# Kernel tuning notes

Hardware: AMD Instinct MI355X
Metric: run time of the kernel (lower is better)

The kernel has to match this reference:

```python
import jax, jax.numpy as jnp
import numpy as np

N_NODES = 50000
N_EDGES = 1600000
IN_DIM = 128
HID = 64
EPS = 1e-6


def setup_inputs() -> dict:
    key = jax.random.key(0)
    ks = jax.random.split(key, 12)
    def g(k, shape, scale):
        return jax.random.normal(k, shape, dtype=jnp.float32) * scale
    x = g(ks[0], (N_NODES, IN_DIM), 1.0)
    edge_index = jax.random.randint(ks[1], (2, N_EDGES), 0, N_NODES, dtype=jnp.int64)
    return {
        "x": x,
        "edge_index": edge_index,
        "w0s": g(ks[2], (IN_DIM, HID), 1.0 / np.sqrt(IN_DIM)),
        "w0n": g(ks[3], (IN_DIM, HID), 1.0 / np.sqrt(IN_DIM)),
        "w1s": g(ks[4], (HID, HID), 1.0 / np.sqrt(HID)),
        "w1n": g(ks[5], (HID, HID), 1.0 / np.sqrt(HID)),
        "w2s": g(ks[6], (HID, HID), 1.0 / np.sqrt(HID)),
        "w2n": g(ks[7], (HID, HID), 1.0 / np.sqrt(HID)),
        "mw1": g(ks[8], (HID, 32), 1.0 / np.sqrt(HID)),
        "mb1": jnp.zeros((32,), jnp.float32),
        "mw2": g(ks[9], (32, 1), 1.0 / np.sqrt(32.0)),
        "mb2": jnp.zeros((1,), jnp.float32),
    }


def _uhg_layer(h, src, dst, inv_deg, ws, wn):
    # transform-then-gather (cheaper: GEMM at node granularity, gather at edge granularity)
    msg = (h @ wn)[src]                                    # [E, HID]
    agg = jax.ops.segment_sum(msg, dst, num_segments=N_NODES) * inv_deg  # mean over in-neighbors
    h2 = jax.nn.relu(h @ ws + agg)
    # projective (UHG) normalization: map embedding back onto the unit sphere / projective rep
    return h2 / (jnp.linalg.norm(h2, axis=-1, keepdims=True) + EPS)


def reference(x, edge_index, w0s, w0n, w1s, w1n, w2s, w2n, mw1, mb1, mw2, mb2):
    src, dst = edge_index[0], edge_index[1]
    deg = jax.ops.segment_sum(jnp.ones((N_EDGES,), jnp.float32), dst, num_segments=N_NODES)
    inv_deg = (1.0 / jnp.maximum(deg, 1.0))[:, None]       # [N,1]
    h = _uhg_layer(x, src, dst, inv_deg, w0s, w0n)
    h = _uhg_layer(h, src, dst, inv_deg, w1s, w1n)
    h = _uhg_layer(h, src, dst, inv_deg, w2s, w2n)
    h = jax.nn.relu(h @ mw1 + mb1)                         # [N,32]
    return jax.nn.sigmoid(h @ mw2 + mb2)                   # [N,1]
```

## Files before the change

kernel.cpp:

```cpp
#include <hip/hip_runtime.h>
#include <hip/hip_bf16.h>
#include <math.h>

#define N_NODES 50000
#define N_EDGES 1600000
#define IN_DIM  128
#define HID     64
#define EPB     4096
#define NBLK    391
#define NB      391
#define CAP     8192
static constexpr float EPS = 1e-6f;

typedef __attribute__((ext_vector_type(8))) short          short8;
typedef __attribute__((ext_vector_type(8))) unsigned short ushort8;
typedef __attribute__((ext_vector_type(4))) float          f32x4;
typedef __attribute__((ext_vector_type(2))) float          f32x2;

__device__ __forceinline__ float bf2f(unsigned int hi_bits) {
    union { unsigned int i; float f; } c; c.i = hi_bits; return c.f;
}
__device__ __forceinline__ unsigned short f2bf(float f) {
    union { float f; unsigned int i; } c; c.f = f;
    unsigned int r = c.i + 0x7FFFu + ((c.i >> 16) & 1u);
    return (unsigned short)(r >> 16);
}
__device__ __forceinline__ unsigned char f2fp8(float f) {
    int p = __builtin_amdgcn_cvt_pk_fp8_f32(f, f, 0, false);
    return (unsigned char)(p & 0xff);
}


template <int K>
__device__ __forceinline__ void pack_body(const float* __restrict__ wS,
                                          const float* __restrict__ wN,
                                          unsigned short* __restrict__ pS,
                                          unsigned short* __restrict__ pN, int blk) {
    constexpr int NSLOT = (K / 32) * 4 * 64;
    int slot = blk * 256 + (int)threadIdx.x;
    if (slot >= NSLOT) return;
    int lane = slot & 63;
    int ct   = slot >> 6;
    int t    = ct & 3;
    int c    = ct >> 2;
    int m    = lane & 15;
    int quad = lane >> 4;
    int col  = t * 16 + m;
#pragma unroll
    for (int j = 0; j < 8; ++j) {
        int k = c * 32 + quad * 8 + j;
        pS[slot * 8 + j] = f2bf(wS[k * 64 + col]);
        pN[slot * 8 + j] = f2bf(wN[k * 64 + col]);
    }
}


__global__ __launch_bounds__(256) void bucket_count_pack(
    const int* __restrict__ ei, int* __restrict__ blockCounts,
    const float* __restrict__ w0s, const float* __restrict__ w0n,
    const float* __restrict__ w1s, const float* __restrict__ w1n,
    const float* __restrict__ w2s, const float* __restrict__ w2n,
    unsigned short* __restrict__ p0S, unsigned short* __restrict__ p0N,
    unsigned short* __restrict__ p1S, unsigned short* __restrict__ p1N,
    unsigned short* __restrict__ p2S, unsigned short* __restrict__ p2N,
    unsigned char* __restrict__ hnq) {
    if (blockIdx.x >= NBLK) {
        int blk = blockIdx.x - NBLK;
        if (blk == 7 && threadIdx.x >= 128 && threadIdx.x < 144)
            ((unsigned int*)(hnq + (size_t)N_NODES * HID))[threadIdx.x - 128] = 0u;
        if (blk < 4)      pack_body<IN_DIM>(w0s, w0n, p0S, p0N, blk);
        else if (blk < 6) pack_body<HID>(w1s, w1n, p1S, p1N, blk - 4);
        else              pack_body<HID>(w2s, w2n, p2S, p2N, blk - 6);
        return;
    }
    __shared__ int hist[NB];
    for (int i = threadIdx.x; i < NB; i += 256) hist[i] = 0;
    __syncthreads();
    int base = blockIdx.x * EPB;
    int lim  = min(EPB, N_EDGES - base);
    for (int i = threadIdx.x; i < lim; i += 256)
        atomicAdd(&hist[ei[N_EDGES + base + i] >> 7], 1);
    __syncthreads();
    for (int b = threadIdx.x; b < NB; b += 256)
        blockCounts[blockIdx.x * NB + b] = hist[b];
}

template <int K, bool F32IN>
__device__ __forceinline__ void gemm_body(
    const void* __restrict__ Av,
    const unsigned short* __restrict__ pS,
    const unsigned short* __restrict__ pN,
    float* __restrict__ hs, unsigned char* __restrict__ hnq, int blk) {
    constexpr int NC = K / 32;
    int lane = threadIdx.x & 63;
    int wv   = threadIdx.x >> 6;
    int tile = blk * 4 + wv;
    if (tile >= N_NODES / 16) return;
    int m    = lane & 15;
    int quad = lane >> 4;

    const short8* pSf = (const short8*)pS;
    const short8* pNf = (const short8*)pN;

    f32x4 accS[4], accN[4];
#pragma unroll
    for (int t = 0; t < 4; ++t) {
        accS[t] = (f32x4){0.f, 0.f, 0.f, 0.f};
        accN[t] = (f32x4){0.f, 0.f, 0.f, 0.f};
    }
#pragma unroll
    for (int c = 0; c < NC; ++c) {
        short8 a;
        if constexpr (F32IN) {
            const float* Af = (const float*)Av + ((size_t)tile * 16 + m) * K + quad * 8 + c * 32;
            f32x4 a0 = *(const f32x4*)Af;
            f32x4 a1 = *(const f32x4*)(Af + 4);
#pragma unroll
            for (int k = 0; k < 4; ++k) a[k]     = (short)f2bf(a0[k]);
#pragma unroll
            for (int k = 0; k < 4; ++k) a[k + 4] = (short)f2bf(a1[k]);
        } else {
            const short8* Af = (const short8*)((const unsigned short*)Av +
                               ((size_t)tile * 16 + m) * K + quad * 8);
            a = Af[c * 4];
        }
#pragma unroll
        for (int t = 0; t < 4; ++t) {
            short8 bs = pSf[(c * 4 + t) * 64 + lane];
            short8 bn = pNf[(c * 4 + t) * 64 + lane];
            accS[t] = __builtin_amdgcn_mfma_f32_16x16x32_bf16(a, bs, accS[t], 0, 0, 0);
            accN[t] = __builtin_amdgcn_mfma_f32_16x16x32_bf16(a, bn, accN[t], 0, 0, 0);
        }
    }
    int row0 = tile * 16 + quad * 4;
#pragma unroll
    for (int t = 0; t < 4; ++t) {
#pragma unroll
        for (int r = 0; r < 4; ++r) {
            size_t o = (size_t)(row0 + r) * HID + t * 16 + m;
            hs[o]  = accS[t][r];
            hnq[o] = f2fp8(accN[t][r]);
        }
    }
}

__global__ __launch_bounds__(256) void col_sum_gemm0(
    const int* __restrict__ blockCounts, int* __restrict__ totals,
    const float* __restrict__ x,
    const unsigned short* __restrict__ p0S, const unsigned short* __restrict__ p0N,
    float* __restrict__ hs, unsigned char* __restrict__ hnq) {
    if (blockIdx.x >= NB) {
        gemm_body<IN_DIM, true>(x, p0S, p0N, hs, hnq, blockIdx.x - NB);
        return;
    }
    __shared__ int ws[4];
    int b = blockIdx.x;
    int s = 0;
    for (int i = threadIdx.x; i < NBLK; i += 256) s += blockCounts[i * NB + b];
#pragma unroll
    for (int off = 32; off >= 1; off >>= 1) s += __shfl_xor(s, off, 64);
    if ((threadIdx.x & 63) == 0) ws[threadIdx.x >> 6] = s;
    __syncthreads();
    if (threadIdx.x == 0) totals[b] = ws[0] + ws[1] + ws[2] + ws[3];
}

__global__ __launch_bounds__(256) void col_fix_base(int* __restrict__ blockCounts,
                                                    const int* __restrict__ totals,
                                                    int* __restrict__ bucketBase) {
    __shared__ int vals[NBLK];
    __shared__ int sbase;
    int b = blockIdx.x;
    for (int i = threadIdx.x; i < NBLK; i += 256) vals[i] = blockCounts[i * NB + b];
    if (threadIdx.x < 64) {
        int lane = threadIdx.x;
        int s = 0;
        for (int i = lane; i < b; i += 64) s += totals[i];
#pragma unroll
        for (int off = 32; off >= 1; off >>= 1) s += __shfl_xor(s, off, 64);
        if (lane == 0) {
            sbase = s;
            bucketBase[b] = s;
            if (b == NB - 1) bucketBase[NB] = s + totals[b];
        }
    }
    __syncthreads();
    if (threadIdx.x < 64) {
        int lane  = threadIdx.x;
        int carry = sbase;
        for (int base = 0; base < NBLK; base += 64) {
            int i = base + lane;
            int v = (i < NBLK) ? vals[i] : 0;
            int incl = v;
#pragma unroll
            for (int off = 1; off < 64; off <<= 1) {
                int t = __shfl_up(incl, off, 64);
                if (lane >= off) incl += t;
            }
            if (i < NBLK) vals[i] = carry + incl - v;
            carry += __shfl(incl, 63, 64);
        }
    }
    __syncthreads();
    for (int i = threadIdx.x; i < NBLK; i += 256) blockCounts[i * NB + b] = vals[i];
}

__global__ __launch_bounds__(256) void bucket_scatter(const int* __restrict__ ei,
                                                      const int* __restrict__ blockCounts,
                                                      unsigned int* __restrict__ bucketPacked) {
    __shared__ int cur[NB];
    for (int b = threadIdx.x; b < NB; b += 256)
        cur[b] = blockCounts[blockIdx.x * NB + b];
    __syncthreads();
    int base = blockIdx.x * EPB;
    int lim  = min(EPB, N_EDGES - base);
    for (int i = threadIdx.x; i < lim; i += 256) {
        int s = ei[base + i];
        int d = ei[N_EDGES + base + i];
        int pos = atomicAdd(&cur[d >> 7], 1);
        bucketPacked[pos] = ((unsigned int)s << 7) | (unsigned int)(d & 127);
    }
}

__global__ __launch_bounds__(256) void node_scan_scatter(
    const unsigned int* __restrict__ bucketPacked, const int* __restrict__ bucketBase,
    int* __restrict__ rowptr, int* __restrict__ csr_src) {
    __shared__ int cnt[128];
    __shared__ int half0;
    __shared__ unsigned int stage[CAP];
    int tid = threadIdx.x;
    if (tid < 128) cnt[tid] = 0;
    __syncthreads();
    int beg = bucketBase[blockIdx.x], end = bucketBase[blockIdx.x + 1];
    int n = end - beg;
    for (int i = tid; i < n; i += 256) {
        unsigned int e = bucketPacked[beg + i];
        if (i < CAP) stage[i] = e;
        atomicAdd(&cnt[e & 127], 1);
    }
    __syncthreads();
    int lane = tid & 63;
    int v    = (tid < 128) ? cnt[tid] : 0;
    int incl = v;
#pragma unroll
    for (int off = 1; off < 64; off <<= 1) {
        int t = __shfl_up(incl, off, 64);
        if (lane >= off) incl += t;
    }
    if (tid == 63) half0 = incl;
    __syncthreads();
    int base  = beg + ((tid >= 64 && tid < 128) ? half0 : 0);
    int start = base + incl - v;
    int node  = blockIdx.x * 128 + tid;
    if (tid < 128) {
        if (node < N_NODES) rowptr[node] = start;
        cnt[tid] = start;
    }
    if (blockIdx.x == 0 && tid == 128) rowptr[N_NODES] = N_EDGES;
    __syncthreads();
    for (int i = tid; i < n; i += 256) {
        unsigned int e = (i < CAP) ? stage[i] : bucketPacked[beg + i];
        int pos = atomicAdd(&cnt[e & 127], 1);
        csr_src[pos] = (int)(e >> 7);
    }
}

template <int K, bool F32IN>
__global__ __launch_bounds__(256) void gemm_dual_mfma(
    const void* __restrict__ Av,
    const unsigned short* __restrict__ pS,
    const unsigned short* __restrict__ pN,
    float* __restrict__ hs, unsigned char* __restrict__ hnq) {
    gemm_body<K, F32IN>(Av, pS, pN, hs, hnq, blockIdx.x);
}

template <bool MLP>
__global__ __launch_bounds__(256) void agg_update(
    const int* __restrict__ rowptr, const int* __restrict__ csr_src,
    const unsigned char* __restrict__ hnq, const float* __restrict__ hs,
    unsigned short* __restrict__ hb_out,
    const float* __restrict__ mw1, const float* __restrict__ mb1,
    const float* __restrict__ mw2, const float* __restrict__ mb2,
    float* __restrict__ out) {
    __shared__ float sW1[MLP ? HID * 32 : 1];
    __shared__ float sW2[MLP ? 32 : 1];
    __shared__ float sB1[MLP ? 32 : 1];
    __shared__ float sH[MLP ? 32 * 68 : 1];
    if (MLP) {
        for (int i = threadIdx.x; i < HID * 32; i += 256) sW1[i] = mw1[i];
        if (threadIdx.x < 32) { sW2[threadIdx.x] = mw2[threadIdx.x]; sB1[threadIdx.x] = mb1[threadIdx.x]; }
        __syncthreads();
    }
    int wid   = blockIdx.x * 4 + (threadIdx.x >> 6);
    int lane  = threadIdx.x & 63;
    int grp   = lane >> 3;
    int r     = lane & 7;
    int node  = wid * 8 + grp;
    bool valid = node < N_NODES;
    int nclamp = valid ? node : 0;
    int beg = rowptr[nclamp];
    int end = rowptr[nclamp + 1];
    int deg = end - beg;
    const unsigned char* hnqB = hnq;
    unsigned r8 = (unsigned)(r * 8);

    f32x2 acc2[4];
#pragma unroll
    for (int k = 0; k < 4; ++k) acc2[k] = (f32x2){0.f, 0.f};

    for (int t = 0; t < deg; t += 8) {
        const int* ip = csr_src + beg + t;
        int si[8];
#pragma unroll
        for (int u = 0; u < 8; ++u) {
            int vraw = ip[u];
            si[u] = (t + u < deg) ? vraw : N_NODES;
        }
        uint2 w[8];
#pragma unroll
        for (int u = 0; u < 8; ++u) {
            unsigned off = ((unsigned)si[u] << 6) | r8;
            w[u] = *(const uint2*)(hnqB + off);
        }
#pragma unroll
        for (int u = 0; u < 8; ++u) {
#if __has_builtin(__builtin_amdgcn_cvt_pk_f32_fp8)
            acc2[0] += __builtin_amdgcn_cvt_pk_f32_fp8((int)w[u].x, false);
            acc2[1] += __builtin_amdgcn_cvt_pk_f32_fp8((int)w[u].x, true);
            acc2[2] += __builtin_amdgcn_cvt_pk_f32_fp8((int)w[u].y, false);
            acc2[3] += __builtin_amdgcn_cvt_pk_f32_fp8((int)w[u].y, true);
#else
            acc2[0] += (f32x2){__builtin_amdgcn_cvt_f32_fp8((int)w[u].x, 0),
                               __builtin_amdgcn_cvt_f32_fp8((int)w[u].x, 1)};
            acc2[1] += (f32x2){__builtin_amdgcn_cvt_f32_fp8((int)w[u].x, 2),
                               __builtin_amdgcn_cvt_f32_fp8((int)w[u].x, 3)};
            acc2[2] += (f32x2){__builtin_amdgcn_cvt_f32_fp8((int)w[u].y, 0),
                               __builtin_amdgcn_cvt_f32_fp8((int)w[u].y, 1)};
            acc2[3] += (f32x2){__builtin_amdgcn_cvt_f32_fp8((int)w[u].y, 2),
                               __builtin_amdgcn_cvt_f32_fp8((int)w[u].y, 3)};
#endif
        }
    }

    float acc[8];
#pragma unroll
    for (int k = 0; k < 4; ++k) { acc[2 * k] = acc2[k][0]; acc[2 * k + 1] = acc2[k][1]; }
    float invdeg = 1.0f / fmaxf((float)deg, 1.0f);
    const float* hsr = hs + (size_t)nclamp * HID + r * 8;
    f32x4 h0 = *(const f32x4*)hsr;
    f32x4 h1 = *(const f32x4*)(hsr + 4);
    float v[8], ss = 0.f;
#pragma unroll
    for (int k = 0; k < 8; ++k) {
        float hk = (k < 4) ? h0[k] : h1[k - 4];
        v[k] = fmaxf(fmaf(acc[k], invdeg, hk), 0.f);
        ss += v[k] * v[k];
    }
    ss += __shfl_xor(ss, 1, 64);
    ss += __shfl_xor(ss, 2, 64);
    ss += __shfl_xor(ss, 4, 64);
    float rs = 1.0f / (sqrtf(ss) + EPS);
    if (MLP) {
        int sn = threadIdx.x >> 3;
#pragma unroll
        for (int k = 0; k < 8; ++k) sH[sn * 68 + r * 8 + k] = v[k] * rs;
        __syncthreads();
        int c0 = r * 4;
        float y0 = sB1[c0], y1 = sB1[c0 + 1], y2 = sB1[c0 + 2], y3 = sB1[c0 + 3];
        const float* hrow = &sH[sn * 68];
#pragma unroll 8
        for (int k = 0; k < HID; ++k) {
            float hv = hrow[k];
            const float* wrow = &sW1[k * 32 + c0];
            y0 = fmaf(hv, wrow[0], y0);
            y1 = fmaf(hv, wrow[1], y1);
            y2 = fmaf(hv, wrow[2], y2);
            y3 = fmaf(hv, wrow[3], y3);
        }
        float p = fmaxf(y0, 0.f) * sW2[c0] + fmaxf(y1, 0.f) * sW2[c0 + 1] +
                  fmaxf(y2, 0.f) * sW2[c0 + 2] + fmaxf(y3, 0.f) * sW2[c0 + 3];
        p += __shfl_xor(p, 1, 64);
        p += __shfl_xor(p, 2, 64);
        p += __shfl_xor(p, 4, 64);
        if (r == 0 && valid) out[node] = 1.0f / (1.0f + __expf(-(p + mb2[0])));
    } else {
        if (valid) {
            ushort8 o;
#pragma unroll
            for (int k = 0; k < 8; ++k) o[k] = f2bf(v[k] * rs);
            *(ushort8*)(hb_out + (size_t)node * HID + r * 8) = o;
        }
    }
}

extern "C" void kernel_launch(void* const* d_in, const int* in_sizes, int n_in,
                              void* d_out, int out_size, void* d_ws, size_t ws_size,
                              hipStream_t stream) {
    const float* x   = (const float*)d_in[0];
    const int*   ei  = (const int*)d_in[1];
    const float* w0s = (const float*)d_in[2];
    const float* w0n = (const float*)d_in[3];
    const float* w1s = (const float*)d_in[4];
    const float* w1n = (const float*)d_in[5];
    const float* w2s = (const float*)d_in[6];
    const float* w2n = (const float*)d_in[7];
    const float* mw1 = (const float*)d_in[8];
    const float* mb1 = (const float*)d_in[9];
    const float* mw2 = (const float*)d_in[10];
    const float* mb2 = (const float*)d_in[11];
    float*       out = (float*)d_out;

    int* rowptr      = (int*)d_ws;
    int* csr_src     = rowptr + 50432;
    int* blockCounts = csr_src + N_EDGES;
    int* bucketBase  = blockCounts + 153600;
    int* totals      = bucketBase + 512;
    unsigned int* bucketPacked = (unsigned int*)(totals + 512);
    const size_t NH = (size_t)N_NODES * HID;
    float*          hs  = (float*)(bucketPacked + N_EDGES);
    unsigned char*  hnq = (unsigned char*)(hs + NH);
    unsigned short* hb  = (unsigned short*)(hnq + NH + 64);
    unsigned short* p0S = hb + NH;
    unsigned short* p0N = p0S + IN_DIM * HID;
    unsigned short* p1S = p0N + IN_DIM * HID;
    unsigned short* p1N = p1S + HID * HID;
    unsigned short* p2S = p1N + HID * HID;
    unsigned short* p2N = p2S + HID * HID;

    const int nodeGrid = (N_NODES / 8 + 3) / 4;
    const int gemmGrid = (N_NODES / 16 + 3) / 4;

    bucket_count_pack<<<NBLK + 8, 256, 0, stream>>>(
        ei, blockCounts, w0s, w0n, w1s, w1n, w2s, w2n,
        p0S, p0N, p1S, p1N, p2S, p2N, hnq);
    col_sum_gemm0<<<NB + gemmGrid, 256, 0, stream>>>(
        blockCounts, totals, x, p0S, p0N, hs, hnq);
    col_fix_base<<<NB, 256, 0, stream>>>(blockCounts, totals, bucketBase);
    bucket_scatter<<<NBLK, 256, 0, stream>>>(ei, blockCounts, bucketPacked);
    node_scan_scatter<<<NB, 256, 0, stream>>>(bucketPacked, bucketBase, rowptr, csr_src);

    agg_update<false><<<nodeGrid, 256, 0, stream>>>(
        rowptr, csr_src, hnq, hs, hb, nullptr, nullptr, nullptr, nullptr, nullptr);

    gemm_dual_mfma<HID, false><<<gemmGrid, 256, 0, stream>>>(hb, p1S, p1N, hs, hnq);
    agg_update<false><<<nodeGrid, 256, 0, stream>>>(
        rowptr, csr_src, hnq, hs, hb, nullptr, nullptr, nullptr, nullptr, nullptr);

    gemm_dual_mfma<HID, false><<<gemmGrid, 256, 0, stream>>>(hb, p2S, p2N, hs, hnq);
    agg_update<true><<<nodeGrid, 256, 0, stream>>>(
        rowptr, csr_src, hnq, hs, nullptr, mw1, mb1, mw2, mb2, out);
}
```

Baseline: 221.6 us.

## Use 16 lanes per node with 4-byte gathers and vectorized aligned index loads

Reworks the aggregation kernel to assign 16 threads per node instead of 8. Each thread gathers 4 fp8 features per neighbor instead of 8. Neighbor indices are now read as aligned 16-byte vectors starting from an 8-aligned base, with out-of-range entries masked to a dummy node. The intent is more parallelism per node and fewer scalar index loads, at the cost of twice as many threads, narrower per-lane gather loads, and an extra shuffle step. The grid now assumes N_NODES is divisible by 16, so the bounds checks are dropped.

```diff
diff --git a/kernel.cpp b/kernel.cpp
--- a/kernel.cpp
+++ b/kernel.cpp
@@ -14,6 +14,8 @@
 
 typedef __attribute__((ext_vector_type(8))) short          short8;
 typedef __attribute__((ext_vector_type(8))) unsigned short ushort8;
+typedef __attribute__((ext_vector_type(4))) unsigned short bf16x4_t;
+typedef __attribute__((ext_vector_type(4))) int            i32x4;
 typedef __attribute__((ext_vector_type(4))) float          f32x4;
 typedef __attribute__((ext_vector_type(2))) float          f32x2;
 
@@ -284,111 +286,95 @@
     __shared__ float sW1[MLP ? HID * 32 : 1];
     __shared__ float sW2[MLP ? 32 : 1];
     __shared__ float sB1[MLP ? 32 : 1];
-    __shared__ float sH[MLP ? 32 * 68 : 1];
+    __shared__ float sH[MLP ? 16 * 68 : 1];
     if (MLP) {
         for (int i = threadIdx.x; i < HID * 32; i += 256) sW1[i] = mw1[i];
         if (threadIdx.x < 32) { sW2[threadIdx.x] = mw2[threadIdx.x]; sB1[threadIdx.x] = mb1[threadIdx.x]; }
         __syncthreads();
     }
-    int wid   = blockIdx.x * 4 + (threadIdx.x >> 6);
-    int lane  = threadIdx.x & 63;
-    int grp   = lane >> 3;
-    int r     = lane & 7;
-    int node  = wid * 8 + grp;
-    bool valid = node < N_NODES;
-    int nclamp = valid ? node : 0;
-    int beg = rowptr[nclamp];
-    int end = rowptr[nclamp + 1];
+    int sn   = threadIdx.x >> 4;
+    int r    = threadIdx.x & 15;
+    int node = blockIdx.x * 16 + sn;
+    int beg = rowptr[node];
+    int end = rowptr[node + 1];
     int deg = end - beg;
-    const unsigned char* hnqB = hnq;
-    unsigned r8 = (unsigned)(r * 8);
-
-    f32x2 acc2[4];
-#pragma unroll
-    for (int k = 0; k < 4; ++k) acc2[k] = (f32x2){0.f, 0.f};
-
-    for (int t = 0; t < deg; t += 8) {
-        const int* ip = csr_src + beg + t;
+    int tbase = beg & ~7;
+    int nbat  = (end - tbase + 7) >> 3;
+    const i32x4* ip = (const i32x4*)(csr_src + tbase);
+    const unsigned char* hrow = hnq + r * 4;
+
+    f32x2 acc2[2];
+    acc2[0] = (f32x2){0.f, 0.f};
+    acc2[1] = (f32x2){0.f, 0.f};
+    int pr = tbase - beg;
+
+#pragma unroll 2
+    for (int t = 0; t < nbat; ++t) {
+        i32x4 a = ip[2 * t];
+        i32x4 b = ip[2 * t + 1];
+        int p0 = pr + 8 * t;
         int si[8];
 #pragma unroll
-        for (int u = 0; u < 8; ++u) {
-            int vraw = ip[u];
-            si[u] = (t + u < deg) ? vraw : N_NODES;
-        }
-        uint2 w[8];
-#pragma unroll
-        for (int u = 0; u < 8; ++u) {
-            unsigned off = ((unsigned)si[u] << 6) | r8;
-            w[u] = *(const uint2*)(hnqB + off);
-        }
+        for (int u = 0; u < 4; ++u) {
+            si[u]     = ((unsigned)(p0 + u)     < (unsigned)deg) ? a[u] : N_NODES;
+            si[u + 4] = ((unsigned)(p0 + 4 + u) < (unsigned)deg) ? b[u] : N_NODES;
+        }
+        unsigned wv[8];
+#pragma unroll
+        for (int u = 0; u < 8; ++u)
+            wv[u] = *(const unsigned*)(hrow + ((unsigned)si[u] << 6));
 #pragma unroll
         for (int u = 0; u < 8; ++u) {
 #if __has_builtin(__builtin_amdgcn_cvt_pk_f32_fp8)
-            acc2[0] += __builtin_amdgcn_cvt_pk_f32_fp8((int)w[u].x, false);
-            acc2[1] += __builtin_amdgcn_cvt_pk_f32_fp8((int)w[u].x, true);
-            acc2[2] += __builtin_amdgcn_cvt_pk_f32_fp8((int)w[u].y, false);
-            acc2[3] += __builtin_amdgcn_cvt_pk_f32_fp8((int)w[u].y, true);
+            acc2[0] += __builtin_amdgcn_cvt_pk_f32_fp8((int)wv[u], false);
+            acc2[1] += __builtin_amdgcn_cvt_pk_f32_fp8((int)wv[u], true);
 #else
-            acc2[0] += (f32x2){__builtin_amdgcn_cvt_f32_fp8((int)w[u].x, 0),
-                               __builtin_amdgcn_cvt_f32_fp8((int)w[u].x, 1)};
-            acc2[1] += (f32x2){__builtin_amdgcn_cvt_f32_fp8((int)w[u].x, 2),
-                               __builtin_amdgcn_cvt_f32_fp8((int)w[u].x, 3)};
-            acc2[2] += (f32x2){__builtin_amdgcn_cvt_f32_fp8((int)w[u].y, 0),
-                               __builtin_amdgcn_cvt_f32_fp8((int)w[u].y, 1)};
-            acc2[3] += (f32x2){__builtin_amdgcn_cvt_f32_fp8((int)w[u].y, 2),
-                               __builtin_amdgcn_cvt_f32_fp8((int)w[u].y, 3)};
+            acc2[0] += (f32x2){__builtin_amdgcn_cvt_f32_fp8((int)wv[u], 0),
+                               __builtin_amdgcn_cvt_f32_fp8((int)wv[u], 1)};
+            acc2[1] += (f32x2){__builtin_amdgcn_cvt_f32_fp8((int)wv[u], 2),
+                               __builtin_amdgcn_cvt_f32_fp8((int)wv[u], 3)};
 #endif
         }
     }
 
-    float acc[8];
-#pragma unroll
-    for (int k = 0; k < 4; ++k) { acc[2 * k] = acc2[k][0]; acc[2 * k + 1] = acc2[k][1]; }
+    float acc[4] = {acc2[0][0], acc2[0][1], acc2[1][0], acc2[1][1]};
     float invdeg = 1.0f / fmaxf((float)deg, 1.0f);
-    const float* hsr = hs + (size_t)nclamp * HID + r * 8;
-    f32x4 h0 = *(const f32x4*)hsr;
-    f32x4 h1 = *(const f32x4*)(hsr + 4);
-    float v[8], ss = 0.f;
-#pragma unroll
-    for (int k = 0; k < 8; ++k) {
-        float hk = (k < 4) ? h0[k] : h1[k - 4];
-        v[k] = fmaxf(fmaf(acc[k], invdeg, hk), 0.f);
+    f32x4 h = *(const f32x4*)(hs + (size_t)node * HID + r * 4);
+    float v[4], ss = 0.f;
+#pragma unroll
+    for (int k = 0; k < 4; ++k) {
+        v[k] = fmaxf(fmaf(acc[k], invdeg, h[k]), 0.f);
         ss += v[k] * v[k];
     }
     ss += __shfl_xor(ss, 1, 64);
     ss += __shfl_xor(ss, 2, 64);
     ss += __shfl_xor(ss, 4, 64);
+    ss += __shfl_xor(ss, 8, 64);
     float rs = 1.0f / (sqrtf(ss) + EPS);
     if (MLP) {
-        int sn = threadIdx.x >> 3;
-#pragma unroll
-        for (int k = 0; k < 8; ++k) sH[sn * 68 + r * 8 + k] = v[k] * rs;
+#pragma unroll
+        for (int k = 0; k < 4; ++k) sH[sn * 68 + r * 4 + k] = v[k] * rs;
         __syncthreads();
-        int c0 = r * 4;
-        float y0 = sB1[c0], y1 = sB1[c0 + 1], y2 = sB1[c0 + 2], y3 = sB1[c0 + 3];
-        const float* hrow = &sH[sn * 68];
+        int c0 = r * 2;
+        float y0 = sB1[c0], y1 = sB1[c0 + 1];
+        const float* hrow2 = &sH[sn * 68];
 #pragma unroll 8
         for (int k = 0; k < HID; ++k) {
-            float hv = hrow[k];
-            const float* wrow = &sW1[k * 32 + c0];
-            y0 = fmaf(hv, wrow[0], y0);
-            y1 = fmaf(hv, wrow[1], y1);
-            y2 = fmaf(hv, wrow[2], y2);
-            y3 = fmaf(hv, wrow[3], y3);
-        }
-        float p = fmaxf(y0, 0.f) * sW2[c0] + fmaxf(y1, 0.f) * sW2[c0 + 1] +
-                  fmaxf(y2, 0.f) * sW2[c0 + 2] + fmaxf(y3, 0.f) * sW2[c0 + 3];
+            float hv = hrow2[k];
+            y0 = fmaf(hv, sW1[k * 32 + c0], y0);
+            y1 = fmaf(hv, sW1[k * 32 + c0 + 1], y1);
+        }
+        float p = fmaxf(y0, 0.f) * sW2[c0] + fmaxf(y1, 0.f) * sW2[c0 + 1];
         p += __shfl_xor(p, 1, 64);
         p += __shfl_xor(p, 2, 64);
         p += __shfl_xor(p, 4, 64);
-        if (r == 0 && valid) out[node] = 1.0f / (1.0f + __expf(-(p + mb2[0])));
+        p += __shfl_xor(p, 8, 64);
+        if (r == 0) out[node] = 1.0f / (1.0f + __expf(-(p + mb2[0])));
     } else {
-        if (valid) {
-            ushort8 o;
-#pragma unroll
-            for (int k = 0; k < 8; ++k) o[k] = f2bf(v[k] * rs);
-            *(ushort8*)(hb_out + (size_t)node * HID + r * 8) = o;
-        }
+        bf16x4_t o;
+#pragma unroll
+        for (int k = 0; k < 4; ++k) o[k] = f2bf(v[k] * rs);
+        *(bf16x4_t*)(hb_out + (size_t)node * HID + r * 4) = o;
     }
 }
 
@@ -426,7 +412,7 @@
     unsigned short* p2S = p1N + HID * HID;
     unsigned short* p2N = p2S + HID * HID;
 
-    const int nodeGrid = (N_NODES / 8 + 3) / 4;
+    const int nodeGrid = N_NODES / 16;
     const int gemmGrid = (N_NODES / 16 + 3) / 4;
 
     bucket_count_pack<<<NBLK + 8, 256, 0, stream>>>(
```

After: 223.6 us. About the same (+0.9%).
